# Optimization experiments

Hardware: AMD Instinct MI355X
Metric: run time of the kernel (lower is better)

Reference implementation:

```python
import jax, jax.numpy as jnp
import numpy as np

C = 128
NUM_GROUPS = 32
EPS = 1e-6


def setup_inputs() -> dict:
    key = jax.random.key(0)
    ks = jax.random.split(key, 6)
    B, H, W = 8, 64, 64
    x = jax.random.normal(ks[0], (B, C, H, W), dtype=jnp.float32)
    # 1x1 conv weights stored as [out_c, in_c] (kernel spatial dims are 1)
    fan_avg = C  # fan_in == fan_out == C for 1x1 conv
    bound = np.sqrt(3.0 / fan_avg)
    wq = jax.random.uniform(ks[1], (C, C), jnp.float32, -bound, bound)
    wk = jax.random.uniform(ks[2], (C, C), jnp.float32, -bound, bound)
    wv = jax.random.uniform(ks[3], (C, C), jnp.float32, -bound, bound)
    # proj_out has init_scale=0.0 -> near-zero init; use tiny random instead to test math
    wo = jax.random.uniform(ks[4], (C, C), jnp.float32, -bound, bound) * 1e-3
    bq = jnp.zeros((C,), jnp.float32)
    bk = jnp.zeros((C,), jnp.float32)
    bv = jnp.zeros((C,), jnp.float32)
    bo = jnp.zeros((C,), jnp.float32)
    gamma = jnp.ones((C,), jnp.float32)
    beta = jnp.zeros((C,), jnp.float32)
    return {"x": x, "gamma": gamma, "beta": beta,
            "wq": wq, "bq": bq, "wk": wk, "bk": bk,
            "wv": wv, "bv": bv, "wo": wo, "bo": bo}


def _group_norm(x, gamma, beta):
    B, Ch, H, W = x.shape
    g = NUM_GROUPS
    xg = x.reshape(B, g, Ch // g, H, W)
    mean = jnp.mean(xg, axis=(2, 3, 4), keepdims=True)
    var = jnp.var(xg, axis=(2, 3, 4), keepdims=True)
    xn = ((xg - mean) * jax.lax.rsqrt(var + EPS)).reshape(B, Ch, H, W)
    return xn * gamma[None, :, None, None] + beta[None, :, None, None]


def _conv1x1(x, w, b):
    # x: [B,C,H,W], w: [O,C], b: [O]
    return jnp.einsum('bchw,oc->bohw', x, w) + b[None, :, None, None]


def reference(x, gamma, beta, wq, bq, wk, bk, wv, bv, wo, bo):
    B, Ch, H, W = x.shape
    n = H * W
    h = _group_norm(x, gamma, beta)
    q = _conv1x1(h, wq, bq).reshape(B, Ch, n)
    k = _conv1x1(h, wk, bk).reshape(B, Ch, n)
    v = _conv1x1(h, wv, bv).reshape(B, Ch, n)
    # attn[b, i, j] = sum_c q[b,c,i] * k[b,c,j] / sqrt(C)
    attn = jnp.einsum('bci,bcj->bij', q, k) * (float(Ch) ** -0.5)
    attn = jax.nn.softmax(attn, axis=-1)
    # h[b,c,i] = sum_j v[b,c,j] * attn[b,i,j]
    out = jnp.einsum('bcj,bij->bci', v, attn).reshape(B, Ch, H, W)
    out = _conv1x1(out, wo, bo)
    return x + out
```

## Files before the change

kernel.cpp:

```cpp
#include <hip/hip_runtime.h>


typedef float f32x4 __attribute__((ext_vector_type(4)));
typedef short short8 __attribute__((ext_vector_type(8)));
typedef _Float16 half8 __attribute__((ext_vector_type(8)));
typedef _Float16 half2t __attribute__((ext_vector_type(2)));
typedef unsigned short ush;
typedef unsigned short ush4 __attribute__((ext_vector_type(4)));
typedef unsigned int uint4t __attribute__((ext_vector_type(4)));
typedef int int8v __attribute__((ext_vector_type(8)));

union V8U {
  uint4t h[2];
  int8v v;
};

__device__ __forceinline__ ush f2bf(float f) {
  unsigned u = __builtin_bit_cast(unsigned, f);
  u = (u + 0x7FFFu + ((u >> 16) & 1u)) >> 16;
  return (ush)u;
}
__device__ __forceinline__ float bf2f(ush v) {
  unsigned u = ((unsigned)v) << 16;
  return __builtin_bit_cast(float, u);
}
__device__ __forceinline__ unsigned f2fp8(float x) {
  unsigned u = __builtin_bit_cast(unsigned, x);
  unsigned s = (u >> 24) & 0x80u;
  unsigned au = u & 0x7fffffffu;
  if (au < 0x3A800000u) return s;
  if (au >= 0x43E00000u) return s | 0x7Eu;
  int e = (int)(au >> 23) - 127;
  if (e < -6) {
    float a = __builtin_bit_cast(float, au);
    int m = (int)(a * 512.0f + 0.5f);
    if (m >= 8) return s | 0x08u;
    return s | (unsigned)m;
  }
  unsigned keep = au >> 20, rem = au & 0xFFFFFu;
  keep += (rem > 0x80000u) || ((rem == 0x80000u) && (keep & 1u));
  int ef = (int)(keep >> 3) - 127;
  if (ef >= 8 && ((ef > 8) || ((keep & 7u) == 7u))) return s | 0x7Eu;
  return s | (unsigned)(((ef + 7) << 3) | (int)(keep & 7u));
}
__device__ __forceinline__ void async16(const void* g, void* l) {
  __builtin_amdgcn_global_load_lds(
      (const __attribute__((address_space(1))) unsigned int*)g,
      (__attribute__((address_space(3))) unsigned int*)l, 16, 0, 0);
}

__global__ __launch_bounds__(256) void gn_stats_kernel(
    const float* __restrict__ x, const float* __restrict__ gamma,
    const float* __restrict__ beta, const float* __restrict__ wo,
    float* __restrict__ scale_c, float* __restrict__ shift_c,
    ush* __restrict__ wob) {
  int bg = blockIdx.x;
  int b = bg >> 5, g = bg & 31;
  int tid = threadIdx.x;
  if (bg < 16) {
    int v4 = (bg * 256 + tid) * 4;
    float4 w4 = *(const float4*)(wo + v4);
    ush4 pk;
    pk.x = f2bf(w4.x); pk.y = f2bf(w4.y);
    pk.z = f2bf(w4.z); pk.w = f2bf(w4.w);
    *(ush4*)(wob + v4) = pk;
  }
  const float4* base = (const float4*)(x + (size_t)bg * 16384);
  float s = 0.f, sq = 0.f;
#pragma unroll
  for (int p = 0; p < 16; ++p) {
    float4 v = base[p * 256 + tid];
    s += (v.x + v.y) + (v.z + v.w);
    sq += (v.x * v.x + v.y * v.y) + (v.z * v.z + v.w * v.w);
  }
#pragma unroll
  for (int off = 32; off > 0; off >>= 1) {
    s += __shfl_down(s, off);
    sq += __shfl_down(sq, off);
  }
  __shared__ float rs[4], rq[4], mv[2];
  int w = tid >> 6, lane = tid & 63;
  if (lane == 0) { rs[w] = s; rq[w] = sq; }
  __syncthreads();
  if (tid == 0) {
    float S = (rs[0] + rs[1]) + (rs[2] + rs[3]);
    float Q = (rq[0] + rq[1]) + (rq[2] + rq[3]);
    float mean = S * (1.f / 16384.f);
    float var = Q * (1.f / 16384.f) - mean * mean;
    mv[0] = mean;
    mv[1] = rsqrtf(var + 1e-6f);
  }
  __syncthreads();
  if (tid < 4) {
    int c = (g << 2) + tid;
    float sc = mv[1] * gamma[c];
    scale_c[(b << 7) + c] = sc;
    shift_c[(b << 7) + c] = beta[c] - mv[0] * sc;
  }
}

__global__ __launch_bounds__(256) void qkv_kernel(
    const float* __restrict__ x, const float* __restrict__ scale_c,
    const float* __restrict__ shift_c, const float* __restrict__ wq,
    const float* __restrict__ wk, const float* __restrict__ wv,
    const float* __restrict__ bq, const float* __restrict__ bk,
    const float* __restrict__ bv, char* __restrict__ Qt8,
    char* __restrict__ Kt8, _Float16* __restrict__ Vh) {
  __shared__ __align__(16) ush hs[64 * 136];
  __shared__ __align__(16) ush wol[128 * 136];
  char* hs8 = (char*)hs;
  int bx = blockIdx.x;
  int type = bx >> 9;
  int rb = bx & 511;
  int b = rb >> 6, i0 = (rb & 63) << 6;
  int tid = threadIdx.x;
  int w = tid >> 6, lane = tid & 63, ln15 = lane & 15, quad = lane >> 4;

#pragma unroll
  for (int p = 0; p < 8; ++p) {
    int id = p * 256 + tid;
    int i = id & 63;
    int g8 = id >> 6;
    int c0 = g8 << 2;
    const float* xp = x + (((size_t)((b << 7) + c0)) << 12) + i0 + i;
    ush4 pk4;
#pragma unroll
    for (int e = 0; e < 4; ++e) {
      float h = xp[(size_t)e << 12] * scale_c[(b << 7) + c0 + e] +
                shift_c[(b << 7) + c0 + e];
      pk4[e] = f2bf(h);
    }
    int pg = g8 ^ ((i & 15) << 1);
    *(ush4*)(hs8 + i * 272 + pg * 8) = pk4;
  }
  const float* W = type == 0 ? wq : (type == 1 ? wk : wv);
#pragma unroll
  for (int p = 0; p < 16; ++p) {
    int v = p * 256 + tid;
    int o = v >> 5, cv = (v & 31) << 2;
    float4 w4 = *(const float4*)(W + (o << 7) + cv);
    uint2 pk;
    pk.x = (unsigned)f2bf(w4.x) | ((unsigned)f2bf(w4.y) << 16);
    pk.y = (unsigned)f2bf(w4.z) | ((unsigned)f2bf(w4.w) << 16);
    *(uint2*)&wol[o * 136 + cv] = pk;
  }
  __syncthreads();

#define HS_FRAG(row, dc) \
  (*(const short8*)(hs8 + (row) * 272 + (((((dc)*4 + quad)) ^ ((row)&15)) << 4)))

  if (type < 2) {
    f32x4 acc[8] = {};
    int hrow = w * 16 + ln15;
#pragma unroll
    for (int dc = 0; dc < 4; ++dc) {
      short8 af = HS_FRAG(hrow, dc);
#pragma unroll
      for (int nb = 0; nb < 8; ++nb) {
        short8 bf = *(const short8*)&wol[(nb * 16 + ln15) * 136 + dc * 32 + quad * 8];
        acc[nb] = __builtin_amdgcn_mfma_f32_16x16x32_bf16(af, bf, acc[nb], 0, 0, 0);
      }
    }
    const float* bias = type == 0 ? bq : bk;
    char* dst8 = type == 0 ? Qt8 : Kt8;
    __syncthreads();
#pragma unroll
    for (int nb = 0; nb < 8; ++nb) {
      int o = nb * 16 + ln15;
      float bi = bias[o];
#pragma unroll
      for (int r = 0; r < 4; ++r) {
        float val = acc[nb][r] + bi;
        if (type == 0) val *= 0.12751742f;
        hs8[(w * 16 + quad * 4 + r) * 144 + o] = (char)f2fp8(val);
      }
    }
    __syncthreads();
    int i = tid >> 2, seg = tid & 3;
    uint4 d0 = *(const uint4*)(hs8 + i * 144 + seg * 32);
    uint4 d1 = *(const uint4*)(hs8 + i * 144 + seg * 32 + 16);
    char* drow = dst8 + (((size_t)((b << 12) + i0 + i)) << 7) + seg * 32;
    *(uint4*)drow = d0;
    *(uint4*)(drow + 16) = d1;
  } else {
    f32x4 acc[8] = {};
    int hrow = w * 16 + ln15;
#pragma unroll
    for (int dc = 0; dc < 4; ++dc) {
      short8 bf = HS_FRAG(hrow, dc);
#pragma unroll
      for (int mb = 0; mb < 8; ++mb) {
        short8 af = *(const short8*)&wol[(mb * 16 + ln15) * 136 + dc * 32 + quad * 8];
        acc[mb] = __builtin_amdgcn_mfma_f32_16x16x32_bf16(af, bf, acc[mb], 0, 0, 0);
      }
    }
#pragma unroll
    for (int mb = 0; mb < 8; ++mb) {
#pragma unroll
      for (int r = 0; r < 4; ++r) {
        int o = mb * 16 + quad * 4 + r;
        float val = acc[mb][r] + bv[o];
        Vh[(((size_t)((b << 7) + o)) << 12) + i0 + w * 16 + ln15] = (_Float16)val;
      }
    }
  }
#undef HS_FRAG
}

__global__ __launch_bounds__(256, 2) void attn_kernel(
    const char* __restrict__ Qt8, const char* __restrict__ Kt8,
    const _Float16* __restrict__ Vh, ush* __restrict__ po,
    float* __restrict__ lw) {
  __shared__ __align__(16) char ksb[2][4096];
  __shared__ __align__(16) _Float16 vsb[2][4096];
  int bx = blockIdx.x;
  int b = bx & 7, qt = (bx >> 3) & 15, ksid = bx >> 7;
  int tid = threadIdx.x;
  int w = tid >> 6, lane = tid & 63, ln15 = lane & 15, quad = lane >> 4;
  int qbase = (qt << 8) + (w << 6);
  int j0 = ksid << 10;

  int8v qf[4];
#pragma unroll
  for (int ih = 0; ih < 4; ++ih) {
    const char* qrow =
        Qt8 + (((size_t)((b << 12) + qbase + ih * 16 + ln15)) << 7) + quad * 32;
    V8U u;
    u.h[0] = *(const uint4t*)(qrow);
    u.h[1] = *(const uint4t*)(qrow + 16);
    qf[ih] = u.v;
  }

  int kj = (w << 3) + (lane >> 3);
  int kh = (kj & 3) | (((kj >> 3) & 1) << 2);
  int kg = (lane & 7) ^ kh;
  const char* ksrc = Kt8 + (((size_t)((b << 12) + j0 + kj)) << 7) + (kg << 4);
  int d0r = (w << 5) + (lane >> 2);
  int d1r = d0r + 16;
  int vg0 = (lane & 3) ^ (((d0r >> 1) + (d0r >> 3)) & 3);
  int vg1 = (lane & 3) ^ (((d1r >> 1) + (d1r >> 3)) & 3);
  const _Float16* vsrc0 =
      Vh + (((size_t)((b << 7) + d0r)) << 12) + j0 + (vg0 << 3);
  const _Float16* vsrc1 =
      Vh + (((size_t)((b << 7) + d1r)) << 12) + j0 + (vg1 << 3);
  char* kdA = &ksb[0][0] + (w << 10);
  char* kdB = &ksb[1][0] + (w << 10);
  char* vdA0 = (char*)&vsb[0][0] + ((w * 2 + 0) << 10);
  char* vdA1 = (char*)&vsb[0][0] + ((w * 2 + 1) << 10);
  char* vdB0 = (char*)&vsb[1][0] + ((w * 2 + 0) << 10);
  char* vdB1 = (char*)&vsb[1][0] + ((w * 2 + 1) << 10);

  async16(ksrc, kdA);
  async16(vsrc0, vdA0);
  async16(vsrc1, vdA1);
  __syncthreads();

  f32x4 O[4][8] = {};
  float lsum[4] = {0.f, 0.f, 0.f, 0.f};
  const f32x4 SINIT = {-7.2134752f, -7.2134752f, -7.2134752f, -7.2134752f};
  int r0 = ((ln15 >> 2) << 3) + (ln15 & 3), r1 = r0 + 4;
  int hr = (ln15 & 3) | (((ln15 >> 2) & 1) << 2);
  int g0 = ((2 * quad) ^ hr) << 4;
  int g1 = ((2 * quad + 1) ^ hr) << 4;

  for (int jt = 0; jt < 32; ++jt) {
    int buf = jt & 1;
    if (jt + 1 < 32) {
      ksrc += 4096;
      vsrc0 += 32;
      vsrc1 += 32;
      if (buf == 0) {
        async16(ksrc, kdB);
        async16(vsrc0, vdB0);
        async16(vsrc1, vdB1);
      } else {
        async16(ksrc, kdA);
        async16(vsrc0, vdA0);
        async16(vsrc1, vdA1);
      }
    }
    const char* kb = &ksb[buf][0];
    const char* vb = (const char*)&vsb[buf][0];

    V8U ka, kc;
    ka.h[0] = *(const uint4t*)(kb + r0 * 128 + g0);
    ka.h[1] = *(const uint4t*)(kb + r0 * 128 + g1);
    kc.h[0] = *(const uint4t*)(kb + r1 * 128 + g0);
    kc.h[1] = *(const uint4t*)(kb + r1 * 128 + g1);
    f32x4 S[4][2];
#pragma unroll
    for (int ih = 0; ih < 4; ++ih) {
      S[ih][0] = __builtin_amdgcn_mfma_scale_f32_16x16x128_f8f6f4(
          ka.v, qf[ih], SINIT, 0, 0, 0, 0x7F7F7F7F, 0, 0x7F7F7F7F);
      S[ih][1] = __builtin_amdgcn_mfma_scale_f32_16x16x128_f8f6f4(
          kc.v, qf[ih], SINIT, 0, 0, 0, 0x7F7F7F7F, 0, 0x7F7F7F7F);
    }

    half8 pf[4];
#pragma unroll
    for (int ih = 0; ih < 4; ++ih) {
      float p0 = __builtin_amdgcn_exp2f(S[ih][0][0]);
      float p1 = __builtin_amdgcn_exp2f(S[ih][0][1]);
      float p2 = __builtin_amdgcn_exp2f(S[ih][0][2]);
      float p3 = __builtin_amdgcn_exp2f(S[ih][0][3]);
      float p4 = __builtin_amdgcn_exp2f(S[ih][1][0]);
      float p5 = __builtin_amdgcn_exp2f(S[ih][1][1]);
      float p6 = __builtin_amdgcn_exp2f(S[ih][1][2]);
      float p7 = __builtin_amdgcn_exp2f(S[ih][1][3]);
      lsum[ih] += ((p0 + p1) + (p2 + p3)) + ((p4 + p5) + (p6 + p7));
      uint4t pw;
      pw.x = __builtin_bit_cast(unsigned, __builtin_amdgcn_cvt_pkrtz(p0, p1));
      pw.y = __builtin_bit_cast(unsigned, __builtin_amdgcn_cvt_pkrtz(p2, p3));
      pw.z = __builtin_bit_cast(unsigned, __builtin_amdgcn_cvt_pkrtz(p4, p5));
      pw.w = __builtin_bit_cast(unsigned, __builtin_amdgcn_cvt_pkrtz(p6, p7));
      pf[ih] = __builtin_bit_cast(half8, pw);
    }
#pragma unroll
    for (int nb = 0; nb < 8; ++nb) {
      int d = nb * 16 + ln15;
      int sd = ((d >> 1) + (d >> 3)) & 3;
      half8 vf = *(const half8*)(vb + d * 64 + ((quad ^ sd) << 4));
#pragma unroll
      for (int ih = 0; ih < 4; ++ih)
        O[ih][nb] = __builtin_amdgcn_mfma_f32_16x16x32_f16(vf, pf[ih], O[ih][nb], 0, 0, 0);
    }
    __syncthreads();
  }

#pragma unroll
  for (int ih = 0; ih < 4; ++ih) {
    float l = lsum[ih];
    l += __shfl_xor(l, 16);
    l += __shfl_xor(l, 32);
    if (quad == 0) lw[(ksid << 15) + (b << 12) + qbase + ih * 16 + ln15] = l;
    int i = qbase + ih * 16 + ln15;
    size_t rowb = (((size_t)((ksid * 8 + b)) << 12) + i) << 7;
#pragma unroll
    for (int nb = 0; nb < 8; ++nb) {
      ush4 pk;
      pk.x = f2bf(O[ih][nb][0]);
      pk.y = f2bf(O[ih][nb][1]);
      pk.z = f2bf(O[ih][nb][2]);
      pk.w = f2bf(O[ih][nb][3]);
      *(ush4*)(po + rowb + nb * 16 + quad * 4) = pk;
    }
  }
}

__global__ __launch_bounds__(256) void proj_kernel(
    const float* __restrict__ x, const ush* __restrict__ po,
    const float* __restrict__ lw, const ush* __restrict__ wob,
    const float* __restrict__ bo, float* __restrict__ out) {
  int bx = blockIdx.x;
  int b = bx >> 6, i0 = (bx & 63) << 6;
  int tid = threadIdx.x;
  int w = tid >> 6, lane = tid & 63, ln15 = lane & 15, quad = lane >> 4;
  int i = i0 + w * 16 + ln15;
  float rl = 0.f;
#pragma unroll
  for (int s = 0; s < 4; ++s) rl += lw[(s << 15) + (b << 12) + i];
  float rinv = 1.f / rl;

  f32x4 acc[8] = {};
#pragma unroll
  for (int dc = 0; dc < 4; ++dc) {
    float vsum[8] = {0.f, 0.f, 0.f, 0.f, 0.f, 0.f, 0.f, 0.f};
#pragma unroll
    for (int s = 0; s < 4; ++s) {
      short8 pv = *(const short8*)(po + (((size_t)(s * 8 + b)) << 19) +
                                   ((size_t)i << 7) + dc * 32 + quad * 8);
#pragma unroll
      for (int e = 0; e < 8; ++e) vsum[e] += bf2f((ush)pv[e]);
    }
    short8 bfv;
#pragma unroll
    for (int e = 0; e < 8; ++e) bfv[e] = (short)f2bf(vsum[e] * rinv);
#pragma unroll
    for (int mb = 0; mb < 8; ++mb) {
      short8 af = *(const short8*)(wob + ((mb * 16 + ln15) << 7) + dc * 32 +
                                   quad * 8);
      acc[mb] = __builtin_amdgcn_mfma_f32_16x16x32_bf16(af, bfv, acc[mb], 0, 0, 0);
    }
  }
#pragma unroll
  for (int mb = 0; mb < 8; ++mb) {
#pragma unroll
    for (int r = 0; r < 4; ++r) {
      int o = mb * 16 + quad * 4 + r;
      size_t idx = (((size_t)(b << 7) + o) << 12) + i;
      out[idx] = x[idx] + acc[mb][r] + bo[o];
    }
  }
}

extern "C" void kernel_launch(void* const* d_in, const int* in_sizes, int n_in,
                              void* d_out, int out_size, void* d_ws,
                              size_t ws_size, hipStream_t stream) {
  const float* x = (const float*)d_in[0];
  const float* gamma = (const float*)d_in[1];
  const float* beta = (const float*)d_in[2];
  const float* wq = (const float*)d_in[3];
  const float* bq = (const float*)d_in[4];
  const float* wk = (const float*)d_in[5];
  const float* bk = (const float*)d_in[6];
  const float* wv = (const float*)d_in[7];
  const float* bv = (const float*)d_in[8];
  const float* wo = (const float*)d_in[9];
  const float* bo = (const float*)d_in[10];
  float* out = (float*)d_out;

  const size_t NE = (size_t)8 * 4096 * 128;
  char* Qt8 = (char*)d_ws;
  char* Kt8 = Qt8 + NE;
  _Float16* Vh = (_Float16*)(Kt8 + NE);
  ush* po = (ush*)(Vh + NE);
  float* lwp = (float*)(po + 4 * NE);
  float* scale_c = lwp + 4 * 32768;
  float* shift_c = scale_c + 1024;
  ush* wob = (ush*)(shift_c + 1024);

  gn_stats_kernel<<<256, 256, 0, stream>>>(x, gamma, beta, wo, scale_c,
                                           shift_c, wob);
  qkv_kernel<<<1536, 256, 0, stream>>>(x, scale_c, shift_c, wq, wk, wv, bq, bk,
                                       bv, Qt8, Kt8, Vh);
  attn_kernel<<<512, 256, 0, stream>>>(Qt8, Kt8, Vh, po, lwp);
  proj_kernel<<<512, 256, 0, stream>>>(x, po, lwp, wob, bo, out);
}
```

Baseline: 188.7 us.

## Pre-convert QKV weights once, use fp16 partials, split projection over outputs

The gn_stats kernel now converts wq/wk/wv to bf16 and wo to fp16 once, so each of the 1536 qkv blocks no longer converts and stages a 128x128 weight tile in LDS and instead reads bf16 fragments straight from global memory. Attention partial outputs are stored as fp16 instead of bf16, which lets the projection kernel sum them with packed half adds and use the f16 MFMA. The projection grid is doubled so each block handles half of the output channels, trading extra partial reads for more parallelism. Risks are less LDS reuse of the weights (global or L2 fragment loads instead) and fp16 range or precision limits on the summed partials.

```diff
diff --git a/kernel.cpp b/kernel.cpp
--- a/kernel.cpp
+++ b/kernel.cpp
@@ -52,18 +52,31 @@
 __global__ __launch_bounds__(256) void gn_stats_kernel(
     const float* __restrict__ x, const float* __restrict__ gamma,
     const float* __restrict__ beta, const float* __restrict__ wo,
-    float* __restrict__ scale_c, float* __restrict__ shift_c,
-    ush* __restrict__ wob) {
+    const float* __restrict__ wq, const float* __restrict__ wk,
+    const float* __restrict__ wv, float* __restrict__ scale_c,
+    float* __restrict__ shift_c, ush* __restrict__ wobh,
+    ush* __restrict__ wqb, ush* __restrict__ wkb, ush* __restrict__ wvb) {
   int bg = blockIdx.x;
   int b = bg >> 5, g = bg & 31;
   int tid = threadIdx.x;
-  if (bg < 16) {
-    int v4 = (bg * 256 + tid) * 4;
-    float4 w4 = *(const float4*)(wo + v4);
+  if (bg < 64) {
+    int m = bg >> 4;
+    int v4 = ((bg & 15) * 256 + tid) * 4;
+    const float* src = m == 0 ? wo : (m == 1 ? wq : (m == 2 ? wk : wv));
+    float4 w4 = *(const float4*)(src + v4);
     ush4 pk;
-    pk.x = f2bf(w4.x); pk.y = f2bf(w4.y);
-    pk.z = f2bf(w4.z); pk.w = f2bf(w4.w);
-    *(ush4*)(wob + v4) = pk;
+    if (m == 0) {
+      pk.x = __builtin_bit_cast(ush, (_Float16)w4.x);
+      pk.y = __builtin_bit_cast(ush, (_Float16)w4.y);
+      pk.z = __builtin_bit_cast(ush, (_Float16)w4.z);
+      pk.w = __builtin_bit_cast(ush, (_Float16)w4.w);
+      *(ush4*)(wobh + v4) = pk;
+    } else {
+      pk.x = f2bf(w4.x); pk.y = f2bf(w4.y);
+      pk.z = f2bf(w4.z); pk.w = f2bf(w4.w);
+      ush* dst = m == 1 ? wqb : (m == 2 ? wkb : wvb);
+      *(ush4*)(dst + v4) = pk;
+    }
   }
   const float4* base = (const float4*)(x + (size_t)bg * 16384);
   float s = 0.f, sq = 0.f;
@@ -101,13 +114,12 @@
 
 __global__ __launch_bounds__(256) void qkv_kernel(
     const float* __restrict__ x, const float* __restrict__ scale_c,
-    const float* __restrict__ shift_c, const float* __restrict__ wq,
-    const float* __restrict__ wk, const float* __restrict__ wv,
+    const float* __restrict__ shift_c, const ush* __restrict__ wqb,
+    const ush* __restrict__ wkb, const ush* __restrict__ wvb,
     const float* __restrict__ bq, const float* __restrict__ bk,
     const float* __restrict__ bv, char* __restrict__ Qt8,
     char* __restrict__ Kt8, _Float16* __restrict__ Vh) {
   __shared__ __align__(16) ush hs[64 * 136];
-  __shared__ __align__(16) ush wol[128 * 136];
   char* hs8 = (char*)hs;
   int bx = blockIdx.x;
   int type = bx >> 9;
@@ -133,21 +145,13 @@
     int pg = g8 ^ ((i & 15) << 1);
     *(ush4*)(hs8 + i * 272 + pg * 8) = pk4;
   }
-  const float* W = type == 0 ? wq : (type == 1 ? wk : wv);
-#pragma unroll
-  for (int p = 0; p < 16; ++p) {
-    int v = p * 256 + tid;
-    int o = v >> 5, cv = (v & 31) << 2;
-    float4 w4 = *(const float4*)(W + (o << 7) + cv);
-    uint2 pk;
-    pk.x = (unsigned)f2bf(w4.x) | ((unsigned)f2bf(w4.y) << 16);
-    pk.y = (unsigned)f2bf(w4.z) | ((unsigned)f2bf(w4.w) << 16);
-    *(uint2*)&wol[o * 136 + cv] = pk;
-  }
+  const ush* Wb = type == 0 ? wqb : (type == 1 ? wkb : wvb);
   __syncthreads();
 
 #define HS_FRAG(row, dc) \
   (*(const short8*)(hs8 + (row) * 272 + (((((dc)*4 + quad)) ^ ((row)&15)) << 4)))
+#define WB_FRAG(o, dc) \
+  (*(const short8*)&Wb[((o) << 7) + (dc)*32 + quad * 8])
 
   if (type < 2) {
     f32x4 acc[8] = {};
@@ -157,7 +161,7 @@
       short8 af = HS_FRAG(hrow, dc);
 #pragma unroll
       for (int nb = 0; nb < 8; ++nb) {
-        short8 bf = *(const short8*)&wol[(nb * 16 + ln15) * 136 + dc * 32 + quad * 8];
+        short8 bf = WB_FRAG(nb * 16 + ln15, dc);
         acc[nb] = __builtin_amdgcn_mfma_f32_16x16x32_bf16(af, bf, acc[nb], 0, 0, 0);
       }
     }
@@ -190,7 +194,7 @@
       short8 bf = HS_FRAG(hrow, dc);
 #pragma unroll
       for (int mb = 0; mb < 8; ++mb) {
-        short8 af = *(const short8*)&wol[(mb * 16 + ln15) * 136 + dc * 32 + quad * 8];
+        short8 af = WB_FRAG(mb * 16 + ln15, dc);
         acc[mb] = __builtin_amdgcn_mfma_f32_16x16x32_bf16(af, bf, acc[mb], 0, 0, 0);
       }
     }
@@ -205,6 +209,7 @@
     }
   }
 #undef HS_FRAG
+#undef WB_FRAG
 }
 
 __global__ __launch_bounds__(256, 2) void attn_kernel(
@@ -338,10 +343,10 @@
 #pragma unroll
     for (int nb = 0; nb < 8; ++nb) {
       ush4 pk;
-      pk.x = f2bf(O[ih][nb][0]);
-      pk.y = f2bf(O[ih][nb][1]);
-      pk.z = f2bf(O[ih][nb][2]);
-      pk.w = f2bf(O[ih][nb][3]);
+      pk.x = __builtin_bit_cast(ush, (_Float16)O[ih][nb][0]);
+      pk.y = __builtin_bit_cast(ush, (_Float16)O[ih][nb][1]);
+      pk.z = __builtin_bit_cast(ush, (_Float16)O[ih][nb][2]);
+      pk.w = __builtin_bit_cast(ush, (_Float16)O[ih][nb][3]);
       *(ush4*)(po + rowb + nb * 16 + quad * 4) = pk;
     }
   }
@@ -349,44 +354,41 @@
 
 __global__ __launch_bounds__(256) void proj_kernel(
     const float* __restrict__ x, const ush* __restrict__ po,
-    const float* __restrict__ lw, const ush* __restrict__ wob,
+    const float* __restrict__ lw, const ush* __restrict__ wobh,
     const float* __restrict__ bo, float* __restrict__ out) {
   int bx = blockIdx.x;
-  int b = bx >> 6, i0 = (bx & 63) << 6;
+  int oh = bx & 1;
+  int bi = bx >> 1;
+  int b = bi >> 6, i0 = (bi & 63) << 6;
   int tid = threadIdx.x;
   int w = tid >> 6, lane = tid & 63, ln15 = lane & 15, quad = lane >> 4;
   int i = i0 + w * 16 + ln15;
   float rl = 0.f;
 #pragma unroll
   for (int s = 0; s < 4; ++s) rl += lw[(s << 15) + (b << 12) + i];
-  float rinv = 1.f / rl;
-
-  f32x4 acc[8] = {};
+  _Float16 rh = (_Float16)(1.f / rl);
+
+  f32x4 acc[4] = {};
 #pragma unroll
   for (int dc = 0; dc < 4; ++dc) {
-    float vsum[8] = {0.f, 0.f, 0.f, 0.f, 0.f, 0.f, 0.f, 0.f};
-#pragma unroll
-    for (int s = 0; s < 4; ++s) {
-      short8 pv = *(const short8*)(po + (((size_t)(s * 8 + b)) << 19) +
-                                   ((size_t)i << 7) + dc * 32 + quad * 8);
-#pragma unroll
-      for (int e = 0; e < 8; ++e) vsum[e] += bf2f((ush)pv[e]);
-    }
-    short8 bfv;
-#pragma unroll
-    for (int e = 0; e < 8; ++e) bfv[e] = (short)f2bf(vsum[e] * rinv);
-#pragma unroll
-    for (int mb = 0; mb < 8; ++mb) {
-      short8 af = *(const short8*)(wob + ((mb * 16 + ln15) << 7) + dc * 32 +
-                                   quad * 8);
-      acc[mb] = __builtin_amdgcn_mfma_f32_16x16x32_bf16(af, bfv, acc[mb], 0, 0, 0);
-    }
-  }
-#pragma unroll
-  for (int mb = 0; mb < 8; ++mb) {
+    size_t base = ((size_t)i << 7) + dc * 32 + quad * 8;
+    half8 vs = *(const half8*)(po + (((size_t)b) << 19) + base);
+#pragma unroll
+    for (int s = 1; s < 4; ++s)
+      vs = vs + *(const half8*)(po + (((size_t)(s * 8 + b)) << 19) + base);
+    half8 bfv = vs * rh;
+#pragma unroll
+    for (int mb = 0; mb < 4; ++mb) {
+      half8 af = *(const half8*)&wobh[(((oh * 4 + mb) * 16 + ln15) << 7) +
+                                      dc * 32 + quad * 8];
+      acc[mb] = __builtin_amdgcn_mfma_f32_16x16x32_f16(af, bfv, acc[mb], 0, 0, 0);
+    }
+  }
+#pragma unroll
+  for (int mb = 0; mb < 4; ++mb) {
 #pragma unroll
     for (int r = 0; r < 4; ++r) {
-      int o = mb * 16 + quad * 4 + r;
+      int o = (oh * 4 + mb) * 16 + quad * 4 + r;
       size_t idx = (((size_t)(b << 7) + o) << 12) + i;
       out[idx] = x[idx] + acc[mb][r] + bo[o];
     }
@@ -417,12 +419,16 @@
   float* lwp = (float*)(po + 4 * NE);
   float* scale_c = lwp + 4 * 32768;
   float* shift_c = scale_c + 1024;
-  ush* wob = (ush*)(shift_c + 1024);
-
-  gn_stats_kernel<<<256, 256, 0, stream>>>(x, gamma, beta, wo, scale_c,
-                                           shift_c, wob);
-  qkv_kernel<<<1536, 256, 0, stream>>>(x, scale_c, shift_c, wq, wk, wv, bq, bk,
-                                       bv, Qt8, Kt8, Vh);
+  ush* wobh = (ush*)(shift_c + 1024);
+  ush* wqb = wobh + 16384;
+  ush* wkb = wqb + 16384;
+  ush* wvb = wkb + 16384;
+
+  gn_stats_kernel<<<256, 256, 0, stream>>>(x, gamma, beta, wo, wq, wk, wv,
+                                           scale_c, shift_c, wobh, wqb, wkb,
+                                           wvb);
+  qkv_kernel<<<1536, 256, 0, stream>>>(x, scale_c, shift_c, wqb, wkb, wvb, bq,
+                                       bk, bv, Qt8, Kt8, Vh);
   attn_kernel<<<512, 256, 0, stream>>>(Qt8, Kt8, Vh, po, lwp);
-  proj_kernel<<<512, 256, 0, stream>>>(x, po, lwp, wob, bo, out);
-}
+  proj_kernel<<<1024, 256, 0, stream>>>(x, po, lwp, wobh, bo, out);
+}
```

New measurement: 199.8 us. +5.9%, slower.
